# Kernel tuning notes

Measured on AMD Instinct MI355X. Metric: run time of the kernel, lower is better.

## Reference

```python
import jax, jax.numpy as jnp
import numpy as np


def setup_inputs() -> dict:
    key = jax.random.key(0)
    k1, k2, k3 = jax.random.split(key, 3)
    B, C, D, S = 16, 80, 1024, 14  # batch, num_classes, feature dim, conv size
    return {
        "batch_size": B,
        "img_feature_map": jax.random.normal(k1, (B, D, S, S), dtype=jnp.float32),
        "word_features": jax.random.normal(k2, (C, D), dtype=jnp.float32),
        "fc_a_w": jax.random.normal(k3, (D,), dtype=jnp.float32) / np.float32(np.sqrt(D)),
        "fc_a_b": jnp.zeros((), dtype=jnp.float32),
    }


def reference(batch_size, img_feature_map, word_features, fc_a_w, fc_a_b):
    # img_feature_map: [B, D, H, W] -> [B, H, W, D]
    img = jnp.transpose(img_feature_map, (0, 2, 3, 1))
    # class-wise gated feature: tanh(img * word) -> [B, H, W, C, D]
    gated = jnp.tanh(img[:, :, :, None, :] * word_features[None, None, None, :, :])
    # rank-1 linear score: [B, H, W, C]
    scores = jnp.einsum('bhwcd,d->bhwc', gated, fc_a_w) + fc_a_b
    B, H, W, C = scores.shape
    # softmax over spatial positions (H*W) per (batch, class)
    coef = jax.nn.softmax(scores.reshape(B, H * W, C), axis=1).reshape(B, H, W, C)
    # attention-weighted spatial pooling -> [B, C, D]
    return jnp.einsum('bhwc,bhwd->bcd', coef, img)
```

## Files before the change

### kernel.cpp

```cpp
#include <hip/hip_runtime.h>

#define BB 16
#define CC 80
#define DD 1024
#define HW 196
#define NSP (BB * HW)
#define NCH 8
#define DCH 128
#define NCQ 16
#define CPB 5
#define PCL 16
#define TWO_LOG2E 2.8853900817779268f

__global__ __launch_bounds__(256) void scores_k(const float* __restrict__ img,
                                                const float* __restrict__ word,
                                                const float* __restrict__ fa,
                                                float* __restrict__ partial) {
    const int g = blockIdx.x * 256 + threadIdx.x;
    if (g >= NSP) return;
    const int b  = g / HW;
    const int hw = g - b * HW;
    const int d0 = blockIdx.y * DCH;
    const int c0 = blockIdx.z * CPB;

    const float* ip = img + ((size_t)b * DD + d0) * HW + hw;

    float p[CPB];
#pragma unroll
    for (int k = 0; k < CPB; ++k) p[k] = 0.f;

    float ivA[32], ivB[32];

    auto loadq = [&](float* iv, int q) {
        const float* qp = ip + (size_t)q * 32 * HW;
#pragma unroll
        for (int i = 0; i < 32; ++i)
            iv[i] = qp[(size_t)i * HW] * TWO_LOG2E;
    };
    auto compute = [&](const float* iv, int q) {
        const float* fp = fa + d0 + q * 32;
#pragma unroll
        for (int k = 0; k < CPB; ++k) {
            const float* wp = word + (size_t)(c0 + k) * DD + d0 + q * 32;
            float p0 = 0.f, p1 = 0.f;
#pragma unroll
            for (int i = 0; i < 32; i += 2) {
                float y0 = iv[i]     * wp[i];
                float y1 = iv[i + 1] * wp[i + 1];
                float e0 = __builtin_amdgcn_exp2f(y0);
                float e1 = __builtin_amdgcn_exp2f(y1);
                float r0 = __builtin_amdgcn_rcpf(e0 + 1.f);
                float r1 = __builtin_amdgcn_rcpf(e1 + 1.f);
                p0 = fmaf(fp[i],     r0, p0);
                p1 = fmaf(fp[i + 1], r1, p1);
            }
            p[k] += p0 + p1;
        }
    };

    loadq(ivA, 0);
    loadq(ivB, 1);
    compute(ivA, 0);
    loadq(ivA, 2);
    compute(ivB, 1);
    loadq(ivB, 3);
    compute(ivA, 2);
    compute(ivB, 3);

#pragma unroll
    for (int k = 0; k < CPB; ++k)
        partial[(((size_t)b * NCH + blockIdx.y) * CC + (c0 + k)) * HW + hw] = p[k];
}

__global__ __launch_bounds__(256) void softmax_k(const float* __restrict__ partial,
                                                 float* __restrict__ coef) {
    const int bc = blockIdx.x;
    const int b = bc / CC, c = bc - b * CC;
    const int t = threadIdx.x;

    float P = 0.f;
    if (t < HW) {
#pragma unroll
        for (int ch = 0; ch < NCH; ++ch)
            P += partial[(((size_t)b * NCH + ch) * CC + c) * HW + t];
    }
    float x = (t < HW) ? (-TWO_LOG2E) * P : -3.4e38f;

    __shared__ float rmax[4], rsum[4];
    const int wv = t >> 6;

    float m = x;
#pragma unroll
    for (int off = 32; off >= 1; off >>= 1) m = fmaxf(m, __shfl_xor(m, off, 64));
    if ((t & 63) == 0) rmax[wv] = m;
    __syncthreads();
    m = fmaxf(fmaxf(rmax[0], rmax[1]), fmaxf(rmax[2], rmax[3]));

    float e = (t < HW) ? __builtin_amdgcn_exp2f(x - m) : 0.f;
    float s = e;
#pragma unroll
    for (int off = 32; off >= 1; off >>= 1) s += __shfl_xor(s, off, 64);
    if ((t & 63) == 0) rsum[wv] = s;
    __syncthreads();
    s = rsum[0] + rsum[1] + rsum[2] + rsum[3];

    if (t < HW) coef[((size_t)b * CC + c) * HW + t] = e * __builtin_amdgcn_rcpf(s);
}

__global__ __launch_bounds__(256) void pool_k(const float* __restrict__ img,
                                              const float* __restrict__ coef,
                                              float* __restrict__ out) {
    __shared__ float it[64 * HW];
    __shared__ float ct[PCL * HW];
    const int b  = blockIdx.x;
    const int d0 = blockIdx.y * 64;
    const int cg = blockIdx.z * PCL;
    const int t  = threadIdx.x;

    const float4* src = (const float4*)(img + ((size_t)b * DD + d0) * HW);
    float4* dst = (float4*)it;
    for (int j = t; j < 64 * HW / 4; j += 256) dst[j] = src[j];
    const float4* csrc = (const float4*)(coef + ((size_t)b * CC + cg) * HW);
    float4* cdst = (float4*)ct;
    for (int j = t; j < PCL * HW / 4; j += 256) cdst[j] = csrc[j];
    __syncthreads();

    const int d  = t & 63;
    const int cq = t >> 6;
    const float* irow = it + d * HW;
    const float* crow = ct + (cq * 4) * HW;

    float a0 = 0.f, a1 = 0.f, a2 = 0.f, a3 = 0.f;
    for (int h = 0; h < HW; h += 4) {
        float4 iv  = *(const float4*)(irow + h);
        float4 c0v = *(const float4*)(crow + h);
        float4 c1v = *(const float4*)(crow + HW + h);
        float4 c2v = *(const float4*)(crow + 2 * HW + h);
        float4 c3v = *(const float4*)(crow + 3 * HW + h);
        a0 = fmaf(iv.x, c0v.x, fmaf(iv.y, c0v.y, fmaf(iv.z, c0v.z, fmaf(iv.w, c0v.w, a0))));
        a1 = fmaf(iv.x, c1v.x, fmaf(iv.y, c1v.y, fmaf(iv.z, c1v.z, fmaf(iv.w, c1v.w, a1))));
        a2 = fmaf(iv.x, c2v.x, fmaf(iv.y, c2v.y, fmaf(iv.z, c2v.z, fmaf(iv.w, c2v.w, a2))));
        a3 = fmaf(iv.x, c3v.x, fmaf(iv.y, c3v.y, fmaf(iv.z, c3v.z, fmaf(iv.w, c3v.w, a3))));
    }

    float* op = out + ((size_t)b * CC + cg + cq * 4) * DD + d0 + d;
    op[0]      = a0;
    op[DD]     = a1;
    op[2 * DD] = a2;
    op[3 * DD] = a3;
}

extern "C" void kernel_launch(void* const* d_in, const int* in_sizes, int n_in,
                              void* d_out, int out_size, void* d_ws, size_t ws_size,
                              hipStream_t stream) {
    const float* img  = (const float*)d_in[1];
    const float* word = (const float*)d_in[2];
    const float* fa   = (const float*)d_in[3];
    float* out = (float*)d_out;

    float* partial = (float*)d_ws;
    float* coef    = partial + (size_t)BB * NCH * CC * HW;

    scores_k<<<dim3((NSP + 255) / 256, NCH, NCQ), 256, 0, stream>>>(img, word, fa, partial);
    softmax_k<<<BB * CC, 256, 0, stream>>>(partial, coef);
    pool_k<<<dim3(BB, DD / 64, CC / PCL), 256, 0, stream>>>(img, coef, out);
}
```

Measured before the change: 162.9 us.

## Hold full 128-dim image slice in registers and widen classes per block

scores_k now loads all 128 image values for its D-chunk into registers once and loops over 8 classes per block instead of 5. That cuts the number of class-group blocks from 16 to 10 and so reduces repeated image reads. The -2log2e scaling moves into scores_k, and pool_k reads the coefficients through wave-uniform (scalar) global loads instead of staging them in LDS. The 128-float register array risks higher VGPR pressure and lower occupancy, and the class loop is no longer unrolled.

```diff
diff --git a/kernel.cpp b/kernel.cpp
--- a/kernel.cpp
+++ b/kernel.cpp
@@ -7,8 +7,8 @@
 #define NSP (BB * HW)
 #define NCH 8
 #define DCH 128
-#define NCQ 16
-#define CPB 5
+#define CPB 8
+#define NCQ (CC / CPB)
 #define PCL 16
 #define TWO_LOG2E 2.8853900817779268f
 
@@ -25,51 +25,38 @@
 
     const float* ip = img + ((size_t)b * DD + d0) * HW + hw;
 
-    float p[CPB];
+    float iv[DCH];
 #pragma unroll
-    for (int k = 0; k < CPB; ++k) p[k] = 0.f;
+    for (int i = 0; i < DCH; ++i) iv[i] = ip[(size_t)i * HW];
+#pragma unroll
+    for (int i = 0; i < DCH; ++i) iv[i] *= TWO_LOG2E;
 
-    float ivA[32], ivB[32];
+    const float* fp = fa + d0;
+    const size_t pbase = (((size_t)b * NCH + blockIdx.y) * CC + c0) * HW + hw;
 
-    auto loadq = [&](float* iv, int q) {
-        const float* qp = ip + (size_t)q * 32 * HW;
-#pragma unroll
-        for (int i = 0; i < 32; ++i)
-            iv[i] = qp[(size_t)i * HW] * TWO_LOG2E;
-    };
-    auto compute = [&](const float* iv, int q) {
-        const float* fp = fa + d0 + q * 32;
-#pragma unroll
-        for (int k = 0; k < CPB; ++k) {
-            const float* wp = word + (size_t)(c0 + k) * DD + d0 + q * 32;
-            float p0 = 0.f, p1 = 0.f;
-#pragma unroll
-            for (int i = 0; i < 32; i += 2) {
-                float y0 = iv[i]     * wp[i];
-                float y1 = iv[i + 1] * wp[i + 1];
-                float e0 = __builtin_amdgcn_exp2f(y0);
-                float e1 = __builtin_amdgcn_exp2f(y1);
-                float r0 = __builtin_amdgcn_rcpf(e0 + 1.f);
-                float r1 = __builtin_amdgcn_rcpf(e1 + 1.f);
-                p0 = fmaf(fp[i],     r0, p0);
-                p1 = fmaf(fp[i + 1], r1, p1);
-            }
-            p[k] += p0 + p1;
+    for (int k = 0; k < CPB; ++k) {
+        const float* wp = word + (size_t)(c0 + k) * DD + d0;
+        float q0 = 0.f, q1 = 0.f, q2 = 0.f, q3 = 0.f;
+        for (int i = 0; i < DCH; i += 4) {
+            float y0 = iv[i + 0] * wp[i + 0];
+            float y1 = iv[i + 1] * wp[i + 1];
+            float y2 = iv[i + 2] * wp[i + 2];
+            float y3 = iv[i + 3] * wp[i + 3];
+            float e0 = __builtin_amdgcn_exp2f(y0);
+            float e1 = __builtin_amdgcn_exp2f(y1);
+            float e2 = __builtin_amdgcn_exp2f(y2);
+            float e3 = __builtin_amdgcn_exp2f(y3);
+            float r0 = __builtin_amdgcn_rcpf(e0 + 1.f);
+            float r1 = __builtin_amdgcn_rcpf(e1 + 1.f);
+            float r2 = __builtin_amdgcn_rcpf(e2 + 1.f);
+            float r3 = __builtin_amdgcn_rcpf(e3 + 1.f);
+            q0 = fmaf(fp[i + 0], r0, q0);
+            q1 = fmaf(fp[i + 1], r1, q1);
+            q2 = fmaf(fp[i + 2], r2, q2);
+            q3 = fmaf(fp[i + 3], r3, q3);
         }
-    };
-
-    loadq(ivA, 0);
-    loadq(ivB, 1);
-    compute(ivA, 0);
-    loadq(ivA, 2);
-    compute(ivB, 1);
-    loadq(ivB, 3);
-    compute(ivA, 2);
-    compute(ivB, 3);
-
-#pragma unroll
-    for (int k = 0; k < CPB; ++k)
-        partial[(((size_t)b * NCH + blockIdx.y) * CC + (c0 + k)) * HW + hw] = p[k];
+        partial[pbase + (size_t)k * HW] = (-TWO_LOG2E) * ((q0 + q1) + (q2 + q3));
+    }
 }
 
 __global__ __launch_bounds__(256) void softmax_k(const float* __restrict__ partial,
@@ -78,13 +65,14 @@
     const int b = bc / CC, c = bc - b * CC;
     const int t = threadIdx.x;
 
-    float P = 0.f;
+    float x = -3.4e38f;
     if (t < HW) {
+        float P = 0.f;
 #pragma unroll
         for (int ch = 0; ch < NCH; ++ch)
             P += partial[(((size_t)b * NCH + ch) * CC + c) * HW + t];
+        x = P;
     }
-    float x = (t < HW) ? (-TWO_LOG2E) * P : -3.4e38f;
 
     __shared__ float rmax[4], rsum[4];
     const int wv = t >> 6;
@@ -111,7 +99,6 @@
                                               const float* __restrict__ coef,
                                               float* __restrict__ out) {
     __shared__ float it[64 * HW];
-    __shared__ float ct[PCL * HW];
     const int b  = blockIdx.x;
     const int d0 = blockIdx.y * 64;
     const int cg = blockIdx.z * PCL;
@@ -120,30 +107,27 @@
     const float4* src = (const float4*)(img + ((size_t)b * DD + d0) * HW);
     float4* dst = (float4*)it;
     for (int j = t; j < 64 * HW / 4; j += 256) dst[j] = src[j];
-    const float4* csrc = (const float4*)(coef + ((size_t)b * CC + cg) * HW);
-    float4* cdst = (float4*)ct;
-    for (int j = t; j < PCL * HW / 4; j += 256) cdst[j] = csrc[j];
     __syncthreads();
 
-    const int d  = t & 63;
-    const int cq = t >> 6;
+    const int d   = t & 63;
+    const int cq4 = __builtin_amdgcn_readfirstlane(t >> 6) * 4;
     const float* irow = it + d * HW;
-    const float* crow = ct + (cq * 4) * HW;
+    const float* cb = coef + ((size_t)b * CC + cg + cq4) * HW;
 
     float a0 = 0.f, a1 = 0.f, a2 = 0.f, a3 = 0.f;
     for (int h = 0; h < HW; h += 4) {
         float4 iv  = *(const float4*)(irow + h);
-        float4 c0v = *(const float4*)(crow + h);
-        float4 c1v = *(const float4*)(crow + HW + h);
-        float4 c2v = *(const float4*)(crow + 2 * HW + h);
-        float4 c3v = *(const float4*)(crow + 3 * HW + h);
+        float4 c0v = *(const float4*)(cb + h);
+        float4 c1v = *(const float4*)(cb + HW + h);
+        float4 c2v = *(const float4*)(cb + 2 * HW + h);
+        float4 c3v = *(const float4*)(cb + 3 * HW + h);
         a0 = fmaf(iv.x, c0v.x, fmaf(iv.y, c0v.y, fmaf(iv.z, c0v.z, fmaf(iv.w, c0v.w, a0))));
         a1 = fmaf(iv.x, c1v.x, fmaf(iv.y, c1v.y, fmaf(iv.z, c1v.z, fmaf(iv.w, c1v.w, a1))));
         a2 = fmaf(iv.x, c2v.x, fmaf(iv.y, c2v.y, fmaf(iv.z, c2v.z, fmaf(iv.w, c2v.w, a2))));
         a3 = fmaf(iv.x, c3v.x, fmaf(iv.y, c3v.y, fmaf(iv.z, c3v.z, fmaf(iv.w, c3v.w, a3))));
     }
 
-    float* op = out + ((size_t)b * CC + cg + cq * 4) * DD + d0 + d;
+    float* op = out + ((size_t)b * CC + cg + cq4) * DD + d0 + d;
     op[0]      = a0;
     op[DD]     = a1;
     op[2 * DD] = a2;
```

Result: slower. 246.1 us (+51.0%).

## Fuse softmax into pooling kernel and simplify score kernel pipelining

Applied to the files above, without the earlier changes.

Removes the separate softmax kernel: each pooling block now sums the per-chunk partial scores, does the spatial softmax per class with wave shuffles, and writes coefficients straight into shared memory. This drops one launch and the global coef round trip, but the softmax work is repeated for every D-tile block (16x redundant). The score kernel also moves from 5 to 4 classes per block (more z-blocks), replaces the manual double-buffered load/compute schedule with a plain loop, and folds the -2log2e scale into the partial store.

```diff
diff --git a/kernel.cpp b/kernel.cpp
--- a/kernel.cpp
+++ b/kernel.cpp
@@ -7,8 +7,8 @@
 #define NSP (BB * HW)
 #define NCH 8
 #define DCH 128
-#define NCQ 16
-#define CPB 5
+#define CPB 4
+#define NCQ (CC / CPB)
 #define PCL 16
 #define TWO_LOG2E 2.8853900817779268f
 
@@ -29,15 +29,13 @@
 #pragma unroll
     for (int k = 0; k < CPB; ++k) p[k] = 0.f;
 
-    float ivA[32], ivB[32];
-
-    auto loadq = [&](float* iv, int q) {
+    for (int q = 0; q < DCH / 32; ++q) {
+        float iv[32];
         const float* qp = ip + (size_t)q * 32 * HW;
 #pragma unroll
         for (int i = 0; i < 32; ++i)
             iv[i] = qp[(size_t)i * HW] * TWO_LOG2E;
-    };
-    auto compute = [&](const float* iv, int q) {
+
         const float* fp = fa + d0 + q * 32;
 #pragma unroll
         for (int k = 0; k < CPB; ++k) {
@@ -56,79 +54,67 @@
             }
             p[k] += p0 + p1;
         }
-    };
-
-    loadq(ivA, 0);
-    loadq(ivB, 1);
-    compute(ivA, 0);
-    loadq(ivA, 2);
-    compute(ivB, 1);
-    loadq(ivB, 3);
-    compute(ivA, 2);
-    compute(ivB, 3);
+    }
 
 #pragma unroll
     for (int k = 0; k < CPB; ++k)
-        partial[(((size_t)b * NCH + blockIdx.y) * CC + (c0 + k)) * HW + hw] = p[k];
+        partial[(((size_t)b * NCH + blockIdx.y) * CC + (c0 + k)) * HW + hw]
+            = (-TWO_LOG2E) * p[k];
 }
 
-__global__ __launch_bounds__(256) void softmax_k(const float* __restrict__ partial,
-                                                 float* __restrict__ coef) {
-    const int bc = blockIdx.x;
-    const int b = bc / CC, c = bc - b * CC;
-    const int t = threadIdx.x;
-
-    float P = 0.f;
-    if (t < HW) {
-#pragma unroll
-        for (int ch = 0; ch < NCH; ++ch)
-            P += partial[(((size_t)b * NCH + ch) * CC + c) * HW + t];
-    }
-    float x = (t < HW) ? (-TWO_LOG2E) * P : -3.4e38f;
-
-    __shared__ float rmax[4], rsum[4];
-    const int wv = t >> 6;
-
-    float m = x;
-#pragma unroll
-    for (int off = 32; off >= 1; off >>= 1) m = fmaxf(m, __shfl_xor(m, off, 64));
-    if ((t & 63) == 0) rmax[wv] = m;
-    __syncthreads();
-    m = fmaxf(fmaxf(rmax[0], rmax[1]), fmaxf(rmax[2], rmax[3]));
-
-    float e = (t < HW) ? __builtin_amdgcn_exp2f(x - m) : 0.f;
-    float s = e;
-#pragma unroll
-    for (int off = 32; off >= 1; off >>= 1) s += __shfl_xor(s, off, 64);
-    if ((t & 63) == 0) rsum[wv] = s;
-    __syncthreads();
-    s = rsum[0] + rsum[1] + rsum[2] + rsum[3];
-
-    if (t < HW) coef[((size_t)b * CC + c) * HW + t] = e * __builtin_amdgcn_rcpf(s);
-}
-
-__global__ __launch_bounds__(256) void pool_k(const float* __restrict__ img,
-                                              const float* __restrict__ coef,
-                                              float* __restrict__ out) {
+__global__ __launch_bounds__(256) void poolmax_k(const float* __restrict__ img,
+                                                 const float* __restrict__ partial,
+                                                 float* __restrict__ out) {
     __shared__ float it[64 * HW];
     __shared__ float ct[PCL * HW];
     const int b  = blockIdx.x;
     const int d0 = blockIdx.y * 64;
     const int cg = blockIdx.z * PCL;
     const int t  = threadIdx.x;
+    const int w  = t >> 6, l = t & 63;
 
     const float4* src = (const float4*)(img + ((size_t)b * DD + d0) * HW);
     float4* dst = (float4*)it;
     for (int j = t; j < 64 * HW / 4; j += 256) dst[j] = src[j];
-    const float4* csrc = (const float4*)(coef + ((size_t)b * CC + cg) * HW);
-    float4* cdst = (float4*)ct;
-    for (int j = t; j < PCL * HW / 4; j += 256) cdst[j] = csrc[j];
+
+#pragma unroll
+    for (int r = 4 * w; r < 4 * w + 4; ++r) {
+        const int c = cg + r;
+        float x0 = 0.f, x1 = 0.f, x2 = 0.f, x3 = 0.f;
+#pragma unroll
+        for (int ch = 0; ch < NCH; ++ch) {
+            const float* pp = partial + (((size_t)b * NCH + ch) * CC + c) * HW;
+            x0 += pp[l];
+            x1 += pp[l + 64];
+            x2 += pp[l + 128];
+            if (l < HW - 192) x3 += pp[l + 192];
+        }
+        float x3m = (l < HW - 192) ? x3 : -3.4e38f;
+
+        float m = fmaxf(fmaxf(x0, x1), fmaxf(x2, x3m));
+#pragma unroll
+        for (int off = 32; off >= 1; off >>= 1) m = fmaxf(m, __shfl_xor(m, off, 64));
+
+        float e0 = __builtin_amdgcn_exp2f(x0 - m);
+        float e1 = __builtin_amdgcn_exp2f(x1 - m);
+        float e2 = __builtin_amdgcn_exp2f(x2 - m);
+        float e3 = (l < HW - 192) ? __builtin_amdgcn_exp2f(x3 - m) : 0.f;
+
+        float s = ((e0 + e1) + (e2 + e3));
+#pragma unroll
+        for (int off = 32; off >= 1; off >>= 1) s += __shfl_xor(s, off, 64);
+
+        float inv = __builtin_amdgcn_rcpf(s);
+        float* cr = ct + r * HW;
+        cr[l]        = e0 * inv;
+        cr[l + 64]   = e1 * inv;
+        cr[l + 128]  = e2 * inv;
+        if (l < HW - 192) cr[l + 192] = e3 * inv;
+    }
     __syncthreads();
 
-    const int d  = t & 63;
-    const int cq = t >> 6;
-    const float* irow = it + d * HW;
-    const float* crow = ct + (cq * 4) * HW;
+    const float* irow = it + l * HW;
+    const float* crow = ct + (4 * w) * HW;
 
     float a0 = 0.f, a1 = 0.f, a2 = 0.f, a3 = 0.f;
     for (int h = 0; h < HW; h += 4) {
@@ -143,11 +129,11 @@
         a3 = fmaf(iv.x, c3v.x, fmaf(iv.y, c3v.y, fmaf(iv.z, c3v.z, fmaf(iv.w, c3v.w, a3))));
     }
 
-    float* op = out + ((size_t)b * CC + cg + cq * 4) * DD + d0 + d;
-    op[0]      = a0;
-    op[DD]     = a1;
-    op[2 * DD] = a2;
-    op[3 * DD] = a3;
+    float* op = out + ((size_t)b * CC + cg + 4 * w) * DD + d0 + l;
+    op[0]          = a0;
+    op[DD]         = a1;
+    op[2 * (size_t)DD] = a2;
+    op[3 * (size_t)DD] = a3;
 }
 
 extern "C" void kernel_launch(void* const* d_in, const int* in_sizes, int n_in,
@@ -159,9 +145,7 @@
     float* out = (float*)d_out;
 
     float* partial = (float*)d_ws;
-    float* coef    = partial + (size_t)BB * NCH * CC * HW;
 
     scores_k<<<dim3((NSP + 255) / 256, NCH, NCQ), 256, 0, stream>>>(img, word, fa, partial);
-    softmax_k<<<BB * CC, 256, 0, stream>>>(partial, coef);
-    pool_k<<<dim3(BB, DD / 64, CC / PCL), 256, 0, stream>>>(img, coef, out);
+    poolmax_k<<<dim3(BB, DD / 64, CC / PCL), 256, 0, stream>>>(img, partial, out);
 }
```

Result: slower. 181.6 us (+11.5%).
